# Performance work log

Hardware: AMD Instinct MI355X
Metric: run time of the kernel (lower is better)

## Reference

```python
import jax, jax.numpy as jnp
import numpy as np

B, N, F_ = 4, 2048, 512
H = 8
D = F_ // H


def setup_inputs() -> dict:
    key = jax.random.key(0)
    ks = jax.random.split(key, 9)
    s = 1.0 / np.sqrt(F_)
    return {
        "x": jax.random.normal(ks[0], (B, N, F_), dtype=jnp.float32),
        "Wq": jax.random.normal(ks[1], (F_, F_), dtype=jnp.float32) * s,
        "bq": jax.random.normal(ks[2], (F_,), dtype=jnp.float32) * 0.01,
        "Wk": jax.random.normal(ks[3], (F_, F_), dtype=jnp.float32) * s,
        "bk": jax.random.normal(ks[4], (F_,), dtype=jnp.float32) * 0.01,
        "Wv": jax.random.normal(ks[5], (F_, F_), dtype=jnp.float32) * s,
        "bv": jax.random.normal(ks[6], (F_,), dtype=jnp.float32) * 0.01,
        "Wo": jax.random.normal(ks[7], (F_, F_), dtype=jnp.float32) * s,
        "bo": jax.random.normal(ks[8], (F_,), dtype=jnp.float32) * 0.01,
    }


def reference(x, Wq, bq, Wk, bk, Wv, bv, Wo, bo):
    b, n, f = x.shape
    h, d = H, f // H
    # projections -> [b, h, n, d]
    q = (x @ Wq + bq).reshape(b, n, h, d).transpose(0, 2, 1, 3)
    k = (x @ Wk + bk).reshape(b, n, h, d).transpose(0, 2, 1, 3)
    v = (x @ Wv + bv).reshape(b, n, h, d).transpose(0, 2, 1, 3)
    # NOTE: module scales by sqrt(feats), not sqrt(head_dim)
    sqrt_d = jnp.asarray(f, x.dtype) ** 0.5
    score = jax.nn.softmax(jnp.einsum('bhif,bhjf->bhij', q, k) / sqrt_d, axis=-1)
    attn = jnp.einsum('bhij,bhjf->bihf', score, v).reshape(b, n, f)
    return attn @ Wo + bo
```

## Files before the change

### kernel.cpp

```cpp
#include <hip/hip_runtime.h>


typedef _Float16 f16;
typedef _Float16 f16x2 __attribute__((ext_vector_type(2)));
typedef _Float16 f16x4 __attribute__((ext_vector_type(4)));
typedef _Float16 f16x8 __attribute__((ext_vector_type(8)));
typedef float f32x4 __attribute__((ext_vector_type(4)));

#define MFMA16(a, b, c) __builtin_amdgcn_mfma_f32_16x16x32_f16((a), (b), (c), 0, 0, 0)
#if __has_builtin(__builtin_amdgcn_exp2f)
#define EXP2(x) __builtin_amdgcn_exp2f(x)
#else
#define EXP2(x) exp2f(x)
#endif
#define GLLDS16(gp, lp)                                                    \
  __builtin_amdgcn_global_load_lds(                                        \
      (const __attribute__((address_space(1))) unsigned int*)(gp),         \
      (__attribute__((address_space(3))) unsigned int*)(lp), 16, 0, 0)

#define QSCALE 0.0637587f

__global__ __launch_bounds__(256) void k_cvt(const float* __restrict__ x,
                                             f16* __restrict__ xb,
                                             const float* __restrict__ Wq,
                                             const float* __restrict__ Wk,
                                             const float* __restrict__ Wv,
                                             const float* __restrict__ Wo,
                                             f16* __restrict__ wt) {
  __shared__ float tl[32][33];
  const int bid = blockIdx.x;
  if (bid < 2048) {
    int i = bid * 256 + threadIdx.x;
    const float4* xp = (const float4*)x;
    f16x4* op = (f16x4*)xb;
    for (; i < 1048576; i += 524288) {
      float4 v = xp[i];
      f16x4 o = {(f16)v.x, (f16)v.y, (f16)v.z, (f16)v.w};
      op[i] = o;
    }
  } else {
    const int wi = bid - 2048;
    const int w = wi >> 8;
    const int bx = wi & 255;
    const float* W = (w == 0) ? Wq : (w == 1) ? Wk : (w == 2) ? Wv : Wo;
    const int j0 = (bx >> 4) * 32;
    const int k0 = (bx & 15) * 32;
    const int tx = threadIdx.x & 31, ty = threadIdx.x >> 5;
#pragma unroll
    for (int i = 0; i < 32; i += 8)
      tl[ty + i][tx] = W[(size_t)(k0 + ty + i) * 512 + j0 + tx];
    __syncthreads();
#pragma unroll
    for (int i = 0; i < 32; i += 8)
      wt[(size_t)w * 262144 + (size_t)(j0 + ty + i) * 512 + (k0 + tx)] =
          (f16)tl[tx][ty + i];
  }
}

template <int BN, int MODE>
__global__ __launch_bounds__(256) void k_gemm(
    const f16* __restrict__ A, const f16* __restrict__ Wb3,
    const float* __restrict__ bias0, const float* __restrict__ bias1,
    const float* __restrict__ bias2, f16* __restrict__ oQ, f16* __restrict__ oK,
    f16* __restrict__ oV, float* __restrict__ oOut) {
  __shared__ __align__(16) f16 a_lds[128 * 64];
  __shared__ __align__(16) f16 b_lds[BN * 64];
  const int t = threadIdx.x;
  const int lane = t & 63, wid = t >> 6;
  const int l15 = lane & 15, l4 = lane >> 4;
  constexpr int MT = (BN == 128) ? 4 : 2;
  const int mbase = (BN == 128) ? (wid >> 1) * 64 : wid * 32;
  const int nbase = (BN == 128) ? (wid & 1) * 64 : 0;
  const int m0 = blockIdx.x * 128;
  const int by = blockIdx.y;
  const int wsel = (MODE == 0) ? (by >> 2) : 0;
  const int n0l = (MODE == 0) ? ((by & 3) * 128) : (by * (BN == 64 ? 64 : 128));
  const f16* Wt = Wb3 + (size_t)wsel * 262144;

  const int srow = t >> 3;
  const int sswz = ((t & 7) ^ (srow & 7)) * 8;
  const f16* Ag = A + (size_t)(m0 + srow) * 512 + sswz;
  const f16* Bg = Wt + (size_t)(n0l + srow) * 512 + sswz;

  f32x4 acc[MT][4];
  const f32x4 z4 = {0.f, 0.f, 0.f, 0.f};
#pragma unroll
  for (int i = 0; i < MT; i++)
#pragma unroll
    for (int j = 0; j < 4; j++) acc[i][j] = z4;

  for (int k0 = 0; k0 < 512; k0 += 64) {
#pragma unroll
    for (int i = 0; i < 4; i++)
      GLLDS16(Ag + (size_t)i * 16384 + k0, &a_lds[i * 2048 + wid * 512]);
#pragma unroll
    for (int i = 0; i < BN / 32; i++)
      GLLDS16(Bg + (size_t)i * 16384 + k0, &b_lds[i * 2048 + wid * 512]);
    __syncthreads();
#pragma unroll
    for (int ks = 0; ks < 2; ks++) {
      const int rs = ((ks * 4 + l4) ^ (l15 & 7)) * 8;
      f16x8 af[MT], bf[4];
#pragma unroll
      for (int mt = 0; mt < MT; mt++)
        af[mt] = *(const f16x8*)&a_lds[(mbase + mt * 16 + l15) * 64 + rs];
#pragma unroll
      for (int nt = 0; nt < 4; nt++)
        bf[nt] = *(const f16x8*)&b_lds[(nbase + nt * 16 + l15) * 64 + rs];
      __builtin_amdgcn_s_setprio(1);
#pragma unroll
      for (int mt = 0; mt < MT; mt++)
#pragma unroll
        for (int nt = 0; nt < 4; nt++)
          acc[mt][nt] = MFMA16(af[mt], bf[nt], acc[mt][nt]);
      __builtin_amdgcn_s_setprio(0);
    }
    __syncthreads();
  }

  if (MODE == 1) {
#pragma unroll
    for (int mt = 0; mt < MT; mt++)
#pragma unroll
      for (int nt = 0; nt < 4; nt++) {
        const int row = m0 + mbase + mt * 16 + l4 * 4;
        const int col = n0l + nbase + nt * 16 + l15;
        const float bv = bias0[col];
#pragma unroll
        for (int r = 0; r < 4; r++)
          oOut[(size_t)(row + r) * 512 + col] = acc[mt][nt][r] + bv;
      }
  } else {
#pragma unroll
    for (int mt = 0; mt < MT; mt++)
#pragma unroll
      for (int nt = 0; nt < 4; nt++) {
        const int colg = by * 128 + nbase + nt * 16 + l15;
        const int w = colg >> 9, jj = colg & 511;
        const int h = jj >> 6, d = jj & 63;
        const float* bp = (w == 0) ? bias0 : (w == 1) ? bias1 : bias2;
        const float bv = bp[jj];
        const float scl = (w == 0) ? QSCALE : 1.0f;
        const int rowg = m0 + mbase + mt * 16 + l4 * 4;
        const int b = rowg >> 11, nn = rowg & 2047;
        if (w == 2) {
          const size_t vb = ((size_t)(b * 8 + h) * 64 + d) * 2048 + nn;
          f16x4 vs;
#pragma unroll
          for (int r = 0; r < 4; r++) vs[r] = (f16)(acc[mt][nt][r] + bv);
          *(f16x4*)&oV[vb] = vs;
        } else {
          f16* op = (w == 0) ? oQ : oK;
          const size_t base = ((size_t)(b * 8 + h) * 2048 + nn) * 64 + d;
#pragma unroll
          for (int r = 0; r < 4; r++)
            op[base + (size_t)r * 64] = (f16)((acc[mt][nt][r] + bv) * scl);
        }
      }
  }
}

__global__ __launch_bounds__(512, 4) void k_attn(const f16* __restrict__ Q,
                                                 const f16* __restrict__ K,
                                                 const f16* __restrict__ Vt,
                                                 f16* __restrict__ CTX) {
  __shared__ __align__(16) f16 k_lds[2][2][4096];
  __shared__ __align__(16) f16 v_lds[2][2][4096];
  const int t = threadIdx.x, wid = t >> 6, lane = t & 63;
  const int l15 = lane & 15, l4 = lane >> 4;
  const int s = wid >> 2, w4 = wid & 3;
  const int bid = blockIdx.x;
  const int bh = (bid & 7) * 4 + (bid >> 7);
  const int qb = (bid >> 3) & 15;
  const int q0 = qb * 128 + w4 * 32;
  const size_t kvb = (size_t)bh * (2048 * 64);
  const int kv0 = s * 1024;

  f16x8 qf[2][2];
#pragma unroll
  for (int g = 0; g < 2; g++)
#pragma unroll
    for (int ks = 0; ks < 2; ks++)
      qf[g][ks] = *(const f16x8*)&Q[kvb + (size_t)(q0 + g * 16 + l15) * 64 +
                                    ks * 32 + l4 * 8];

  f32x4 oa[2][4];
  f32x4 lacc[2];
  const f32x4 z4 = {0.f, 0.f, 0.f, 0.f};
#pragma unroll
  for (int g = 0; g < 2; g++) {
    lacc[g] = z4;
#pragma unroll
    for (int dt = 0; dt < 4; dt++) oa[g][dt] = z4;
  }
  const f16 one = (f16)1.0f;
  const f16x8 ones = {one, one, one, one, one, one, one, one};

  const int krow = w4 * 8 + (lane >> 3);
  const int kswz = ((lane & 7) ^ (lane >> 3)) * 8;
  const int kperm = ((krow & 0x0C) << 1) | ((krow & 0x10) >> 2) | (krow & 3);
  const f16* Kg = K + kvb + (size_t)(kv0 + kperm) * 64 + kswz;
  const f16* Vg = Vt + kvb + (size_t)krow * 2048 + kv0 + kswz;

  GLLDS16(Kg, &k_lds[s][0][w4 * 512]);
  GLLDS16(Kg + 2048, &k_lds[s][0][w4 * 512 + 2048]);
  GLLDS16(Vg, &v_lds[s][0][w4 * 512]);
  GLLDS16(Vg + 32 * 2048, &v_lds[s][0][w4 * 512 + 2048]);
  __syncthreads();

  int cur = 0;
  for (int it = 0; it < 16; ++it) {
    if (it < 15) {
      const size_t kb = (size_t)(it + 1) * 4096;
      const size_t vb = (size_t)(it + 1) * 64;
      GLLDS16(Kg + kb, &k_lds[s][cur ^ 1][w4 * 512]);
      GLLDS16(Kg + kb + 2048, &k_lds[s][cur ^ 1][w4 * 512 + 2048]);
      GLLDS16(Vg + vb, &v_lds[s][cur ^ 1][w4 * 512]);
      GLLDS16(Vg + vb + 32 * 2048, &v_lds[s][cur ^ 1][w4 * 512 + 2048]);
    }

    f32x4 st[2][4];
#pragma unroll
    for (int g = 0; g < 2; g++)
#pragma unroll
      for (int w = 0; w < 4; w++) st[g][w] = z4;
    const f16* kl = &k_lds[s][cur][0];
#pragma unroll
    for (int ks = 0; ks < 2; ks++) {
      const int rs = ((ks * 4 + l4) ^ (l15 & 7)) * 8;
      f16x8 kf[4];
#pragma unroll
      for (int w = 0; w < 4; w++)
        kf[w] = *(const f16x8*)&kl[(w * 16 + l15) * 64 + rs];
      __builtin_amdgcn_s_setprio(1);
#pragma unroll
      for (int w = 0; w < 4; w++) {
        st[0][w] = MFMA16(kf[w], qf[0][ks], st[0][w]);
        st[1][w] = MFMA16(kf[w], qf[1][ks], st[1][w]);
      }
      __builtin_amdgcn_s_setprio(0);
    }

    f16x8 pa[2][2];
#pragma unroll
    for (int g = 0; g < 2; g++)
#pragma unroll
      for (int ks = 0; ks < 2; ks++) {
        f16x2 a0 = __builtin_bit_cast(
            f16x2, __builtin_amdgcn_cvt_pkrtz(EXP2(st[g][2 * ks][0]),
                                              EXP2(st[g][2 * ks][1])));
        f16x2 a1 = __builtin_bit_cast(
            f16x2, __builtin_amdgcn_cvt_pkrtz(EXP2(st[g][2 * ks][2]),
                                              EXP2(st[g][2 * ks][3])));
        f16x2 a2 = __builtin_bit_cast(
            f16x2, __builtin_amdgcn_cvt_pkrtz(EXP2(st[g][2 * ks + 1][0]),
                                              EXP2(st[g][2 * ks + 1][1])));
        f16x2 a3 = __builtin_bit_cast(
            f16x2, __builtin_amdgcn_cvt_pkrtz(EXP2(st[g][2 * ks + 1][2]),
                                              EXP2(st[g][2 * ks + 1][3])));
        f16x8 p;
        p[0] = a0[0]; p[1] = a0[1]; p[2] = a1[0]; p[3] = a1[1];
        p[4] = a2[0]; p[5] = a2[1]; p[6] = a3[0]; p[7] = a3[1];
        pa[g][ks] = p;
      }

    const f16* vl = &v_lds[s][cur][0];
#pragma unroll
    for (int ks = 0; ks < 2; ks++) {
      __builtin_amdgcn_s_setprio(1);
      lacc[0] = MFMA16(pa[0][ks], ones, lacc[0]);
      lacc[1] = MFMA16(pa[1][ks], ones, lacc[1]);
#pragma unroll
      for (int dt = 0; dt < 4; dt++) {
        const f16x8 vf = *(const f16x8*)&vl[(dt * 16 + l15) * 64 +
                                            ((ks * 4 + l4) ^ (l15 & 7)) * 8];
        oa[0][dt] = MFMA16(pa[0][ks], vf, oa[0][dt]);
        oa[1][dt] = MFMA16(pa[1][ks], vf, oa[1][dt]);
      }
      __builtin_amdgcn_s_setprio(0);
    }
    __syncthreads();
    cur ^= 1;
  }

  float* so = (float*)&k_lds[0][0][0];
  float* sl = (float*)&v_lds[0][0][0];
  const int ln = w4 * 64 + lane;
  if (s == 1) {
#pragma unroll
    for (int g = 0; g < 2; g++) {
#pragma unroll
      for (int dt = 0; dt < 4; dt++)
#pragma unroll
        for (int r = 0; r < 4; r++)
          so[(g * 16 + dt * 4 + r) * 256 + ln] = oa[g][dt][r];
#pragma unroll
      for (int r = 0; r < 4; r++) sl[(g * 4 + r) * 256 + ln] = lacc[g][r];
    }
  }
  __syncthreads();
  if (s == 0) {
    const int b = bh >> 3, h = bh & 7;
#pragma unroll
    for (int g = 0; g < 2; g++) {
#pragma unroll
      for (int r = 0; r < 4; r++) {
        const float lt = lacc[g][r] + sl[(g * 4 + r) * 256 + ln];
        const float inv = 1.0f / lt;
        const int qrow = q0 + g * 16 + l4 * 4 + r;
#pragma unroll
        for (int dt = 0; dt < 4; dt++) {
          const float ov =
              oa[g][dt][r] + so[(g * 16 + dt * 4 + r) * 256 + ln];
          CTX[(size_t)(b * 2048 + qrow) * 512 + h * 64 + dt * 16 + l15] =
              (f16)(ov * inv);
        }
      }
    }
  }
}

extern "C" void kernel_launch(void* const* d_in, const int* in_sizes, int n_in,
                              void* d_out, int out_size, void* d_ws,
                              size_t ws_size, hipStream_t stream) {
  const float* x = (const float*)d_in[0];
  const float* Wq = (const float*)d_in[1];
  const float* bq = (const float*)d_in[2];
  const float* Wk = (const float*)d_in[3];
  const float* bk = (const float*)d_in[4];
  const float* Wv = (const float*)d_in[5];
  const float* bv = (const float*)d_in[6];
  const float* Wo = (const float*)d_in[7];
  const float* bo = (const float*)d_in[8];
  float* out = (float*)d_out;
  char* ws = (char*)d_ws;

  f16* xb = (f16*)(ws);
  f16* wt = (f16*)(ws + (size_t)(8u << 20));
  f16* Qb = (f16*)(ws + (size_t)(10u << 20));
  f16* Kb = (f16*)(ws + (size_t)(18u << 20));
  f16* Vt = (f16*)(ws + (size_t)(26u << 20));
  f16* CX = (f16*)(ws + (size_t)(34u << 20));

  k_cvt<<<dim3(3072), dim3(256), 0, stream>>>(x, xb, Wq, Wk, Wv, Wo, wt);
  k_gemm<128, 0><<<dim3(64, 12), dim3(256), 0, stream>>>(
      xb, wt, bq, bk, bv, Qb, Kb, Vt, nullptr);
  k_attn<<<dim3(512), dim3(512), 0, stream>>>(Qb, Kb, Vt, CX);
  k_gemm<64, 1><<<dim3(64, 8), dim3(256), 0, stream>>>(
      CX, wt + (size_t)3 * 262144, bo, nullptr, nullptr, nullptr, nullptr,
      nullptr, out);
}
```

Before: 80.21 us.

## Switch attention kernel to 32x32x16 MFMA with new K/V LDS layout

The attention kernel now uses 32x32x16 f16 MFMA tiles instead of 16x16x32 for both QK^T and PV. K and V are staged into LDS with a matching permuted layout, which reduces LDS fragment loads per MFMA. The softmax row sum is now computed on the VALU with a cross-half shuffle, replacing the extra MFMA against a ones vector. The trade-off is larger accumulator register footprint per wave, and a final normalization that goes through LDS.

```diff
diff --git a/kernel.cpp b/kernel.cpp
--- a/kernel.cpp
+++ b/kernel.cpp
@@ -6,8 +6,10 @@
 typedef _Float16 f16x4 __attribute__((ext_vector_type(4)));
 typedef _Float16 f16x8 __attribute__((ext_vector_type(8)));
 typedef float f32x4 __attribute__((ext_vector_type(4)));
+typedef float f32x16 __attribute__((ext_vector_type(16)));
 
 #define MFMA16(a, b, c) __builtin_amdgcn_mfma_f32_16x16x32_f16((a), (b), (c), 0, 0, 0)
+#define MFMA32(a, b, c) __builtin_amdgcn_mfma_f32_32x32x16_f16((a), (b), (c), 0, 0, 0)
 #if __has_builtin(__builtin_amdgcn_exp2f)
 #define EXP2(x) __builtin_amdgcn_exp2f(x)
 #else
@@ -167,7 +169,7 @@
   __shared__ __align__(16) f16 k_lds[2][2][4096];
   __shared__ __align__(16) f16 v_lds[2][2][4096];
   const int t = threadIdx.x, wid = t >> 6, lane = t & 63;
-  const int l15 = lane & 15, l4 = lane >> 4;
+  const int l31 = lane & 31, hi = lane >> 5, hi8 = hi * 8;
   const int s = wid >> 2, w4 = wid & 3;
   const int bid = blockIdx.x;
   const int bh = (bid & 7) * 4 + (bid >> 7);
@@ -176,146 +178,140 @@
   const size_t kvb = (size_t)bh * (2048 * 64);
   const int kv0 = s * 1024;
 
-  f16x8 qf[2][2];
-#pragma unroll
-  for (int g = 0; g < 2; g++)
-#pragma unroll
-    for (int ks = 0; ks < 2; ks++)
-      qf[g][ks] = *(const f16x8*)&Q[kvb + (size_t)(q0 + g * 16 + l15) * 64 +
-                                    ks * 32 + l4 * 8];
-
-  f32x4 oa[2][4];
-  f32x4 lacc[2];
-  const f32x4 z4 = {0.f, 0.f, 0.f, 0.f};
-#pragma unroll
-  for (int g = 0; g < 2; g++) {
-    lacc[g] = z4;
-#pragma unroll
-    for (int dt = 0; dt < 4; dt++) oa[g][dt] = z4;
-  }
-  const f16 one = (f16)1.0f;
-  const f16x8 ones = {one, one, one, one, one, one, one, one};
-
-  const int krow = w4 * 8 + (lane >> 3);
-  const int kswz = ((lane & 7) ^ (lane >> 3)) * 8;
-  const int kperm = ((krow & 0x0C) << 1) | ((krow & 0x10) >> 2) | (krow & 3);
-  const f16* Kg = K + kvb + (size_t)(kv0 + kperm) * 64 + kswz;
-  const f16* Vg = Vt + kvb + (size_t)krow * 2048 + kv0 + kswz;
-
-  GLLDS16(Kg, &k_lds[s][0][w4 * 512]);
-  GLLDS16(Kg + 2048, &k_lds[s][0][w4 * 512 + 2048]);
-  GLLDS16(Vg, &v_lds[s][0][w4 * 512]);
-  GLLDS16(Vg + 32 * 2048, &v_lds[s][0][w4 * 512 + 2048]);
+  f16x8 qf[4];
+#pragma unroll
+  for (int s4 = 0; s4 < 4; s4++)
+    qf[s4] = *(const f16x8*)&Q[kvb + (size_t)(q0 + l31) * 64 + s4 * 16 + hi8];
+
+  f32x16 oa0, oa1;
+  const f32x16 z16 = {0.f, 0.f, 0.f, 0.f, 0.f, 0.f, 0.f, 0.f,
+                      0.f, 0.f, 0.f, 0.f, 0.f, 0.f, 0.f, 0.f};
+  oa0 = z16;
+  oa1 = z16;
+  float lacc_s = 0.f;
+
+  const int tl = w4 * 64 + lane;
+  const int kvl = (tl >> 1) & 31;
+  const int Pk = (kvl & 3) | (((kvl >> 4) & 1) << 2) | (((kvl >> 2) & 1) << 3) |
+                 (((kvl >> 3) & 1) << 4);
+  const int kk = w4 * 16 + (tl & 1) * 8;
+  const f16* Kg = K + kvb + (size_t)(kv0 + Pk) * 64 + kk;
+  const int dl = (tl >> 1) & 31;
+  const int kvv = w4 * 16 + (tl & 1) * 8;
+  const f16* Vg = Vt + kvb + (size_t)dl * 2048 + kv0 + kvv;
+
+  {
+    f16* kd = &k_lds[s][0][0] + tl * 8;
+    f16* vd = &v_lds[s][0][0] + tl * 8;
+    GLLDS16(Kg, kd);
+    GLLDS16(Kg + 2048, kd + 2048);
+    GLLDS16(Vg, vd);
+    GLLDS16(Vg + 65536, vd + 2048);
+  }
   __syncthreads();
 
   int cur = 0;
   for (int it = 0; it < 16; ++it) {
     if (it < 15) {
-      const size_t kb = (size_t)(it + 1) * 4096;
-      const size_t vb = (size_t)(it + 1) * 64;
-      GLLDS16(Kg + kb, &k_lds[s][cur ^ 1][w4 * 512]);
-      GLLDS16(Kg + kb + 2048, &k_lds[s][cur ^ 1][w4 * 512 + 2048]);
-      GLLDS16(Vg + vb, &v_lds[s][cur ^ 1][w4 * 512]);
-      GLLDS16(Vg + vb + 32 * 2048, &v_lds[s][cur ^ 1][w4 * 512 + 2048]);
-    }
-
-    f32x4 st[2][4];
-#pragma unroll
-    for (int g = 0; g < 2; g++)
-#pragma unroll
-      for (int w = 0; w < 4; w++) st[g][w] = z4;
+      const size_t ka = (size_t)(it + 1) * 4096;
+      const size_t va = (size_t)(it + 1) * 64;
+      f16* kd = &k_lds[s][cur ^ 1][0] + tl * 8;
+      f16* vd = &v_lds[s][cur ^ 1][0] + tl * 8;
+      GLLDS16(Kg + ka, kd);
+      GLLDS16(Kg + ka + 2048, kd + 2048);
+      GLLDS16(Vg + va, vd);
+      GLLDS16(Vg + va + 65536, vd + 2048);
+    }
+
+    f32x16 st0 = z16, st1 = z16;
     const f16* kl = &k_lds[s][cur][0];
 #pragma unroll
-    for (int ks = 0; ks < 2; ks++) {
-      const int rs = ((ks * 4 + l4) ^ (l15 & 7)) * 8;
-      f16x8 kf[4];
-#pragma unroll
-      for (int w = 0; w < 4; w++)
-        kf[w] = *(const f16x8*)&kl[(w * 16 + l15) * 64 + rs];
+    for (int s4 = 0; s4 < 4; s4++) {
+      const f16x8 kf0 = *(const f16x8*)&kl[s4 * 512 + l31 * 16 + hi8];
+      const f16x8 kf1 = *(const f16x8*)&kl[2048 + s4 * 512 + l31 * 16 + hi8];
       __builtin_amdgcn_s_setprio(1);
-#pragma unroll
-      for (int w = 0; w < 4; w++) {
-        st[0][w] = MFMA16(kf[w], qf[0][ks], st[0][w]);
-        st[1][w] = MFMA16(kf[w], qf[1][ks], st[1][w]);
-      }
+      st0 = MFMA32(kf0, qf[s4], st0);
+      st1 = MFMA32(kf1, qf[s4], st1);
       __builtin_amdgcn_s_setprio(0);
     }
 
-    f16x8 pa[2][2];
-#pragma unroll
-    for (int g = 0; g < 2; g++)
-#pragma unroll
-      for (int ks = 0; ks < 2; ks++) {
-        f16x2 a0 = __builtin_bit_cast(
-            f16x2, __builtin_amdgcn_cvt_pkrtz(EXP2(st[g][2 * ks][0]),
-                                              EXP2(st[g][2 * ks][1])));
-        f16x2 a1 = __builtin_bit_cast(
-            f16x2, __builtin_amdgcn_cvt_pkrtz(EXP2(st[g][2 * ks][2]),
-                                              EXP2(st[g][2 * ks][3])));
-        f16x2 a2 = __builtin_bit_cast(
-            f16x2, __builtin_amdgcn_cvt_pkrtz(EXP2(st[g][2 * ks + 1][0]),
-                                              EXP2(st[g][2 * ks + 1][1])));
-        f16x2 a3 = __builtin_bit_cast(
-            f16x2, __builtin_amdgcn_cvt_pkrtz(EXP2(st[g][2 * ks + 1][2]),
-                                              EXP2(st[g][2 * ks + 1][3])));
-        f16x8 p;
-        p[0] = a0[0]; p[1] = a0[1]; p[2] = a1[0]; p[3] = a1[1];
-        p[4] = a2[0]; p[5] = a2[1]; p[6] = a3[0]; p[7] = a3[1];
-        pa[g][ks] = p;
-      }
+    float e0[16], e1[16];
+#pragma unroll
+    for (int r = 0; r < 16; r++) {
+      e0[r] = EXP2(st0[r]);
+      e1[r] = EXP2(st1[r]);
+    }
+    float sm = 0.f;
+#pragma unroll
+    for (int r = 0; r < 16; r++) sm += e0[r] + e1[r];
+    lacc_s += sm;
+
+    f16x8 pa00, pa01, pa10, pa11;
+    {
+      f16x2 c0, c1, c2, c3;
+#define PK8(dst, e, w)                                                      \
+      c0 = __builtin_bit_cast(                                              \
+          f16x2, __builtin_amdgcn_cvt_pkrtz(e[4 * (w)], e[4 * (w) + 1]));   \
+      c1 = __builtin_bit_cast(                                              \
+          f16x2, __builtin_amdgcn_cvt_pkrtz(e[4 * (w) + 2], e[4 * (w) + 3]));\
+      c2 = __builtin_bit_cast(                                              \
+          f16x2, __builtin_amdgcn_cvt_pkrtz(e[4 * (w) + 8], e[4 * (w) + 9]));\
+      c3 = __builtin_bit_cast(                                              \
+          f16x2,                                                            \
+          __builtin_amdgcn_cvt_pkrtz(e[4 * (w) + 10], e[4 * (w) + 11]));    \
+      dst[0] = c0[0]; dst[1] = c0[1]; dst[2] = c1[0]; dst[3] = c1[1];       \
+      dst[4] = c2[0]; dst[5] = c2[1]; dst[6] = c3[0]; dst[7] = c3[1];
+      PK8(pa00, e0, 0)
+      PK8(pa01, e0, 1)
+      PK8(pa10, e1, 0)
+      PK8(pa11, e1, 1)
+#undef PK8
+    }
 
     const f16* vl = &v_lds[s][cur][0];
-#pragma unroll
-    for (int ks = 0; ks < 2; ks++) {
-      __builtin_amdgcn_s_setprio(1);
-      lacc[0] = MFMA16(pa[0][ks], ones, lacc[0]);
-      lacc[1] = MFMA16(pa[1][ks], ones, lacc[1]);
-#pragma unroll
-      for (int dt = 0; dt < 4; dt++) {
-        const f16x8 vf = *(const f16x8*)&vl[(dt * 16 + l15) * 64 +
-                                            ((ks * 4 + l4) ^ (l15 & 7)) * 8];
-        oa[0][dt] = MFMA16(pa[0][ks], vf, oa[0][dt]);
-        oa[1][dt] = MFMA16(pa[1][ks], vf, oa[1][dt]);
-      }
-      __builtin_amdgcn_s_setprio(0);
-    }
+    const int vb = l31 * 16 + hi8;
+    __builtin_amdgcn_s_setprio(1);
+    oa0 = MFMA32(pa00, *(const f16x8*)&vl[vb], oa0);
+    oa1 = MFMA32(pa00, *(const f16x8*)&vl[2048 + vb], oa1);
+    oa0 = MFMA32(pa01, *(const f16x8*)&vl[512 + vb], oa0);
+    oa1 = MFMA32(pa01, *(const f16x8*)&vl[2560 + vb], oa1);
+    oa0 = MFMA32(pa10, *(const f16x8*)&vl[1024 + vb], oa0);
+    oa1 = MFMA32(pa10, *(const f16x8*)&vl[3072 + vb], oa1);
+    oa0 = MFMA32(pa11, *(const f16x8*)&vl[1536 + vb], oa0);
+    oa1 = MFMA32(pa11, *(const f16x8*)&vl[3584 + vb], oa1);
+    __builtin_amdgcn_s_setprio(0);
     __syncthreads();
     cur ^= 1;
   }
 
+  lacc_s += __shfl_xor(lacc_s, 32);
+
   float* so = (float*)&k_lds[0][0][0];
   float* sl = (float*)&v_lds[0][0][0];
+  float* linv = ((float*)&v_lds[0][0][0]) + 256;
   const int ln = w4 * 64 + lane;
   if (s == 1) {
 #pragma unroll
-    for (int g = 0; g < 2; g++) {
-#pragma unroll
-      for (int dt = 0; dt < 4; dt++)
-#pragma unroll
-        for (int r = 0; r < 4; r++)
-          so[(g * 16 + dt * 4 + r) * 256 + ln] = oa[g][dt][r];
-#pragma unroll
-      for (int r = 0; r < 4; r++) sl[(g * 4 + r) * 256 + ln] = lacc[g][r];
-    }
+    for (int r = 0; r < 16; r++) {
+      so[r * 256 + ln] = oa0[r];
+      so[(16 + r) * 256 + ln] = oa1[r];
+    }
+    sl[ln] = lacc_s;
   }
   __syncthreads();
   if (s == 0) {
+    const float ltot = lacc_s + sl[ln];
+    if (lane < 32) linv[w4 * 32 + l31] = 1.0f / ltot;
     const int b = bh >> 3, h = bh & 7;
 #pragma unroll
-    for (int g = 0; g < 2; g++) {
-#pragma unroll
-      for (int r = 0; r < 4; r++) {
-        const float lt = lacc[g][r] + sl[(g * 4 + r) * 256 + ln];
-        const float inv = 1.0f / lt;
-        const int qrow = q0 + g * 16 + l4 * 4 + r;
-#pragma unroll
-        for (int dt = 0; dt < 4; dt++) {
-          const float ov =
-              oa[g][dt][r] + so[(g * 16 + dt * 4 + r) * 256 + ln];
-          CTX[(size_t)(b * 2048 + qrow) * 512 + h * 64 + dt * 16 + l15] =
-              (f16)(ov * inv);
-        }
-      }
+    for (int r = 0; r < 16; r++) {
+      const int qrow = q0 + (r & 3) + 8 * (r >> 2) + 4 * hi;
+      const float inv = linv[w4 * 32 + ((r & 3) + 8 * (r >> 2) + 4 * hi)];
+      const float v0 = oa0[r] + so[r * 256 + ln];
+      const float v1 = oa1[r] + so[(16 + r) * 256 + ln];
+      const size_t rb = (size_t)(b * 2048 + qrow) * 512 + h * 64;
+      CTX[rb + l31] = (f16)(v0 * inv);
+      CTX[rb + 32 + l31] = (f16)(v1 * inv);
     }
   }
 }
```

New measurement: 83.98 us. 4.7% more time.
